# Kernel optimization log

Measured on AMD Instinct MI355X. Metric: run time of the kernel, lower is better.

The kernel has to match this reference:

```python
import jax, jax.numpy as jnp
import numpy as np

N = 62          # EEG channels (nodes per graph)
B = 512         # graphs in batch
K = 2           # SGConv propagation steps
F_IN = 128
H = 64
C = 3


def _complete_graph_edge_index():
    # edge e = g*N*N + i*N + j connects node g*N+i -> g*N+j,
    # matching edge_weight = Wsym.reshape(-1).repeat(B) ordering.
    base = np.arange(N)
    ii = np.tile(np.repeat(base, N), B)
    jj = np.tile(np.tile(base, N), B)
    off = np.repeat(np.arange(B) * N, N * N)
    return jnp.asarray(np.stack([off + ii, off + jj]).astype(np.int32))


def setup_inputs() -> dict:
    key = jax.random.key(0)
    ks = jax.random.split(key, 6)
    n_total = B * N
    x = jax.random.normal(ks[0], (n_total, F_IN), dtype=jnp.float32)
    edge_weight_tril = jax.random.normal(ks[1], (N * (N + 1) // 2,), dtype=jnp.float32)
    W1 = jax.random.normal(ks[2], (H, F_IN), dtype=jnp.float32) * (1.0 / np.sqrt(F_IN))
    b1 = jax.random.normal(ks[3], (H,), dtype=jnp.float32) * 0.01
    W2 = jax.random.normal(ks[4], (C, H), dtype=jnp.float32) * (1.0 / np.sqrt(H))
    b2 = jax.random.normal(ks[5], (C,), dtype=jnp.float32) * 0.01
    edge_index = _complete_graph_edge_index()
    batch = jnp.asarray(np.repeat(np.arange(B), N).astype(np.int32))
    return {"x": x, "edge_weight_tril": edge_weight_tril, "W1": W1, "b1": b1,
            "W2": W2, "b2": b2, "edge_index": edge_index, "batch": batch,
            "batch_size": B}


def reference(x, edge_weight_tril, W1, b1, W2, b2, edge_index, batch, batch_size):
    n_total = x.shape[0]
    # rebuild symmetric dense adjacency from lower-tri params
    xs, ys = np.tril_indices(N)
    Wm = jnp.zeros((N, N), dtype=x.dtype).at[xs, ys].set(edge_weight_tril)
    Wsym = Wm + Wm.T - jnp.diag(jnp.diag(Wm))
    ew = jnp.tile(Wsym.reshape(-1), batch_size)            # [B*N*N]

    row, col = edge_index[0], edge_index[1]
    # symmetric normalization (graph already contains self loops)
    deg = jax.ops.segment_sum(jnp.abs(ew), row, num_segments=n_total)
    dinv = jnp.where(deg > 0, deg ** -0.5, 0.0)
    norm = dinv[row] * ew * dinv[col]                      # [E]

    # K-step SGConv propagation: gather, scale, scatter-add
    h = x
    for _ in range(K):
        h = jax.ops.segment_sum(norm[:, None] * h[row], col, num_segments=n_total)

    h = jax.nn.relu(h @ W1.T + b1)                         # [n_total, H]
    pooled = jax.ops.segment_sum(h, batch, num_segments=batch_size)  # global_add_pool
    latent_v = pooled                                      # dropout in eval mode = identity
    logits = latent_v @ W2.T + b2
    logp = jax.nn.log_softmax(logits, axis=-1)
    return latent_v, logp
```

## Files before the change

kernel.cpp:

```cpp
#include <hip/hip_runtime.h>
#include <math.h>

#define NN  62
#define BGR 512
#define FIN 128
#define HD  64
#define NC  3

typedef __attribute__((ext_vector_type(8))) short          bf16x8;
typedef __attribute__((ext_vector_type(4))) float          f32x4;
typedef __attribute__((ext_vector_type(4))) unsigned short us4;

static __device__ __forceinline__ unsigned short f2bf(float f) {
    union { float f; unsigned u; } v; v.f = f;
    unsigned u = v.u;
    return (unsigned short)((u + 0x7fffu + ((u >> 16) & 1u)) >> 16);
}
static __device__ __forceinline__ float bf2f(unsigned short h) {
    union { unsigned u; float f; } v; v.u = ((unsigned)h) << 16;
    return v.f;
}

__global__ __launch_bounds__(512) void gcn_all(
    const float* __restrict__ x, const float* __restrict__ tril,
    const float* __restrict__ W1, const float* __restrict__ b1,
    const float* __restrict__ W2, const float* __restrict__ b2,
    float* __restrict__ out) {
    __shared__ unsigned short SH[45056];
    __shared__ float TAIL[2176 + 64 + 64];
    float* partial = TAIL;
    float* b1S     = TAIL + 2176;
    float* dinvS   = TAIL + 2240;

    const int t = threadIdx.x;
    const int gb = blockIdx.x;
    const int lane = t & 63, wv = t >> 6, quad = lane >> 4, l15 = lane & 15;
    const int w4 = wv & 3, gsel = wv >> 2;
    const int graph = 2 * gb + gsel;

    if (t < 16) *(float4*)&b1S[4 * t] = ((const float4*)b1)[t];

    bf16x8 xh[4], xl[4];
    {
        const int xr = 16 * w4 + l15;
        if (xr < NN) {
            const float* xrow = x + (size_t)graph * NN * FIN + (size_t)xr * FIN + quad * 8;
#pragma unroll
            for (int c = 0; c < 4; ++c) {
                float4 a = *(const float4*)(xrow + c * 32);
                float4 b = *(const float4*)(xrow + c * 32 + 4);
                float vv[8] = {a.x, a.y, a.z, a.w, b.x, b.y, b.z, b.w};
#pragma unroll
                for (int k = 0; k < 8; ++k) {
                    unsigned short h = f2bf(vv[k]);
                    xh[c][k] = (short)h;
                    xl[c][k] = (short)f2bf(vv[k] - bf2f(h));
                }
            }
        } else {
            bf16x8 zv = {0, 0, 0, 0, 0, 0, 0, 0};
#pragma unroll
            for (int c = 0; c < 4; ++c) { xh[c] = zv; xl[c] = zv; }
        }
    }

    const int arow_i = 16 * w4 + l15;
    const int jbase  = 16 * quad;
    float wreg[16];
    float dinv_r = 0.f;

    if (gsel == 1) {
        const float4* w14 = (const float4*)W1;
        for (int e = t - 256; e < 2048; e += 256) {
            int h = e >> 5, f4 = e & 31;
            float4 v = w14[e];
            us4 hh, ll;
            hh[0] = f2bf(v.x); ll[0] = f2bf(v.x - bf2f(hh[0]));
            hh[1] = f2bf(v.y); ll[1] = f2bf(v.y - bf2f(hh[1]));
            hh[2] = f2bf(v.z); ll[2] = f2bf(v.z - bf2f(hh[2]));
            hh[3] = f2bf(v.w); ll[3] = f2bf(v.w - bf2f(hh[3]));
            *(us4*)&SH[       h * 136 + f4 * 4] = hh;
            *(us4*)&SH[8704 + h * 136 + f4 * 4] = ll;
        }
    } else {
        float ps = 0.f;
#pragma unroll
        for (int jj = 0; jj < 16; ++jj) {
            int j = jbase + jj;
            float w = 0.f;
            if (arow_i < NN && j < NN) {
                int hi = arow_i > j ? arow_i : j;
                int lo = arow_i > j ? j : arow_i;
                w = tril[hi * (hi + 1) / 2 + lo];
            }
            wreg[jj] = w;
            ps += fabsf(w);
        }
        ps += __shfl_xor(ps, 16);
        ps += __shfl_xor(ps, 32);
        dinv_r = (ps > 0.f) ? (1.0f / sqrtf(ps)) : 0.f;
        if (lane < 16) dinvS[16 * w4 + lane] = dinv_r;
    }
    __syncthreads();

    if (gsel == 0) {
        const float di = dinv_r;
#pragma unroll
        for (int k = 0; k < 4; ++k) {
            float4 d4 = *(float4*)&dinvS[jbase + 4 * k];
            float dja[4] = {d4.x, d4.y, d4.z, d4.w};
            us4 hh, ll;
#pragma unroll
            for (int e = 0; e < 4; ++e) {
                float v = di * wreg[4 * k + e] * dja[e];
                hh[e] = f2bf(v);
                ll[e] = f2bf(v - bf2f(hh[e]));
            }
            *(us4*)&SH[17408 + arow_i * 72 + jbase + 4 * k] = hh;
            *(us4*)&SH[22016 + arow_i * 72 + jbase + 4 * k] = ll;
        }
    }
    __syncthreads();

    f32x4 za0 = {0,0,0,0}, za1 = {0,0,0,0};
    {
        const int arow = 17408 + arow_i * 72 + quad * 8;
        const int nt0 = 2 * gsel;
#pragma unroll
        for (int c = 0; c < 2; ++c) {
            bf16x8 ahi = *(bf16x8*)&SH[arow + c * 32];
            bf16x8 alo = *(bf16x8*)&SH[4608 + arow + c * 32];
#define ATILE(ACC, NT) { \
            int bo = 17408 + (16 * (NT) + l15) * 72 + quad * 8 + c * 32; \
            bf16x8 bhi = *(bf16x8*)&SH[bo]; \
            bf16x8 blo = *(bf16x8*)&SH[4608 + bo]; \
            ACC = __builtin_amdgcn_mfma_f32_16x16x32_bf16(ahi, bhi, ACC, 0, 0, 0); \
            ACC = __builtin_amdgcn_mfma_f32_16x16x32_bf16(ahi, blo, ACC, 0, 0, 0); \
            ACC = __builtin_amdgcn_mfma_f32_16x16x32_bf16(alo, bhi, ACC, 0, 0, 0); }
            ATILE(za0, nt0) ATILE(za1, nt0 + 1)
#undef ATILE
        }
    }

    f32x4 y0 = {0,0,0,0}, y1 = {0,0,0,0}, y2 = {0,0,0,0}, y3 = {0,0,0,0};
    {
#pragma unroll
        for (int c = 0; c < 4; ++c) {
            bf16x8 ahi = xh[c];
            bf16x8 alo = xl[c];
#define P1TILE(ACC, NT) { \
            int bo = (16 * (NT) + l15) * 136 + quad * 8 + c * 32; \
            bf16x8 bhi = *(bf16x8*)&SH[bo]; \
            bf16x8 blo = *(bf16x8*)&SH[8704 + bo]; \
            ACC = __builtin_amdgcn_mfma_f32_16x16x32_bf16(ahi, bhi, ACC, 0, 0, 0); \
            ACC = __builtin_amdgcn_mfma_f32_16x16x32_bf16(ahi, blo, ACC, 0, 0, 0); \
            ACC = __builtin_amdgcn_mfma_f32_16x16x32_bf16(alo, bhi, ACC, 0, 0, 0); }
            P1TILE(y0, 0) P1TILE(y1, 1) P1TILE(y2, 2) P1TILE(y3, 3)
#undef P1TILE
        }
    }
    __syncthreads();

    const int ytbase = 26624 + gsel * 9216;
    {
        const int mbase = 16 * w4 + quad * 4;
#define SPLITW(ACC, NT, HIOFF, LOOFF) { \
        int n = 16 * (NT) + l15; \
        us4 hh, ll; \
        hh[0] = f2bf(ACC[0]); ll[0] = f2bf(ACC[0] - bf2f(hh[0])); \
        hh[1] = f2bf(ACC[1]); ll[1] = f2bf(ACC[1] - bf2f(hh[1])); \
        hh[2] = f2bf(ACC[2]); ll[2] = f2bf(ACC[2] - bf2f(hh[2])); \
        hh[3] = f2bf(ACC[3]); ll[3] = f2bf(ACC[3] - bf2f(hh[3])); \
        *(us4*)&SH[(HIOFF) + n * 72 + mbase] = hh; \
        *(us4*)&SH[(LOOFF) + n * 72 + mbase] = ll; }
        SPLITW(y0, 0, ytbase, ytbase + 4608) SPLITW(y1, 1, ytbase, ytbase + 4608)
        SPLITW(y2, 2, ytbase, ytbase + 4608) SPLITW(y3, 3, ytbase, ytbase + 4608)
        SPLITW(za0, 2 * gsel,     17408, 22016)
        SPLITW(za1, 2 * gsel + 1, 17408, 22016)
#undef SPLITW
    }
    __syncthreads();

    f32x4 z0 = {0,0,0,0}, z1 = {0,0,0,0}, z2 = {0,0,0,0}, z3 = {0,0,0,0};
    {
        const int arow = 17408 + arow_i * 72 + quad * 8;
#pragma unroll
        for (int c = 0; c < 2; ++c) {
            bf16x8 ahi = *(bf16x8*)&SH[arow + c * 32];
            bf16x8 alo = *(bf16x8*)&SH[4608 + arow + c * 32];
#define P2TILE(ACC, NT) { \
            int bo = ytbase + (16 * (NT) + l15) * 72 + quad * 8 + c * 32; \
            bf16x8 bhi = *(bf16x8*)&SH[bo]; \
            bf16x8 blo = *(bf16x8*)&SH[4608 + bo]; \
            ACC = __builtin_amdgcn_mfma_f32_16x16x32_bf16(ahi, bhi, ACC, 0, 0, 0); \
            ACC = __builtin_amdgcn_mfma_f32_16x16x32_bf16(ahi, blo, ACC, 0, 0, 0); \
            ACC = __builtin_amdgcn_mfma_f32_16x16x32_bf16(alo, bhi, ACC, 0, 0, 0); }
            P2TILE(z0, 0) P2TILE(z1, 1) P2TILE(z2, 2) P2TILE(z3, 3)
#undef P2TILE
        }
    }

    {
        const int mbase = 16 * w4 + quad * 4;
        const int slot = 4 * w4 + quad;
        float* part = partial + gsel * 1088;
#define POOL(ACC, NT) { \
        int n = 16 * (NT) + l15; \
        float bn = b1S[n]; \
        float p = 0.f; \
        if (mbase + 0 < 62) p += fmaxf(ACC[0] + bn, 0.f); \
        if (mbase + 1 < 62) p += fmaxf(ACC[1] + bn, 0.f); \
        if (mbase + 2 < 62) p += fmaxf(ACC[2] + bn, 0.f); \
        if (mbase + 3 < 62) p += fmaxf(ACC[3] + bn, 0.f); \
        part[n * 17 + slot] = p; }
        POOL(z0, 0) POOL(z1, 1) POOL(z2, 2) POOL(z3, 3)
#undef POOL
    }
    __syncthreads();

    int tg = -1, tt = 0;
    if (t < 64)                    { tg = 0; tt = t; }
    else if (t >= 256 && t < 320)  { tg = 1; tt = t - 256; }
    if (tg >= 0) {
        const float* part = partial + tg * 1088;
        const int gr = 2 * gb + tg;
        float s = 0.f;
#pragma unroll
        for (int q = 0; q < 16; ++q) s += part[tt * 17 + q];
        out[(size_t)gr * HD + tt] = s;
        float l0 = s * W2[tt];
        float l1 = s * W2[64 + tt];
        float l2 = s * W2[128 + tt];
#pragma unroll
        for (int off = 32; off > 0; off >>= 1) {
            l0 += __shfl_down(l0, off);
            l1 += __shfl_down(l1, off);
            l2 += __shfl_down(l2, off);
        }
        if (tt == 0) {
            l0 += b2[0]; l1 += b2[1]; l2 += b2[2];
            float m = fmaxf(l0, fmaxf(l1, l2));
            float lse = m + logf(expf(l0 - m) + expf(l1 - m) + expf(l2 - m));
            float* lp = out + (size_t)BGR * HD + (size_t)gr * NC;
            lp[0] = l0 - lse; lp[1] = l1 - lse; lp[2] = l2 - lse;
        }
    }
}

extern "C" void kernel_launch(void* const* d_in, const int* in_sizes, int n_in,
                              void* d_out, int out_size, void* d_ws, size_t ws_size,
                              hipStream_t stream) {
    const float* x    = (const float*)d_in[0];
    const float* tril = (const float*)d_in[1];
    const float* W1   = (const float*)d_in[2];
    const float* b1   = (const float*)d_in[3];
    const float* W2   = (const float*)d_in[4];
    const float* b2   = (const float*)d_in[5];
    float* out = (float*)d_out;

    gcn_all<<<BGR / 2, 512, 0, stream>>>(x, tril, W1, b1, W2, b2, out);
}
```

Baseline: 92.88 us.

## Remove a barrier via separate normalized-adjacency buffer, defer x conversion, shuffle-reduce pool

The propagated adjacency now goes to a new LDS region instead of overwriting the normalized A tile. That removes the barrier between the second MFMA phase and the split-writes. The fp32-to-bf16 hi/lo split of x is deferred until after the adjacency/W1 staging, so the global loads can overlap with that work. Pooling partials are reduced across quads with wave shuffles, which replaces the 16-slot LDS reduction. LDS use grows by about 18 KB, which may lower occupancy.

```diff
diff --git a/kernel.cpp b/kernel.cpp
--- a/kernel.cpp
+++ b/kernel.cpp
@@ -26,11 +26,11 @@
     const float* __restrict__ W1, const float* __restrict__ b1,
     const float* __restrict__ W2, const float* __restrict__ b2,
     float* __restrict__ out) {
-    __shared__ unsigned short SH[45056];
-    __shared__ float TAIL[2176 + 64 + 64];
-    float* partial = TAIL;
-    float* b1S     = TAIL + 2176;
-    float* dinvS   = TAIL + 2240;
+    __shared__ unsigned short SH[54272];
+    __shared__ float TAIL[512 + 64 + 64];
+    float* partial2 = TAIL;
+    float* b1S      = TAIL + 512;
+    float* dinvS    = TAIL + 576;
 
     const int t = threadIdx.x;
     const int gb = blockIdx.x;
@@ -40,32 +40,35 @@
 
     if (t < 16) *(float4*)&b1S[4 * t] = ((const float4*)b1)[t];
 
+    const int arow_i = 16 * w4 + l15;
+    float4 xr4[8];
+    {
+        if (arow_i < NN) {
+            const float4* p4 = (const float4*)(x + (size_t)graph * NN * FIN
+                                               + (size_t)arow_i * FIN + quad * 8);
+#pragma unroll
+            for (int c = 0; c < 4; ++c) { xr4[2*c] = p4[8*c]; xr4[2*c+1] = p4[8*c+1]; }
+        } else {
+            float4 zz = {0.f, 0.f, 0.f, 0.f};
+#pragma unroll
+            for (int c = 0; c < 8; ++c) xr4[c] = zz;
+        }
+    }
     bf16x8 xh[4], xl[4];
-    {
-        const int xr = 16 * w4 + l15;
-        if (xr < NN) {
-            const float* xrow = x + (size_t)graph * NN * FIN + (size_t)xr * FIN + quad * 8;
-#pragma unroll
-            for (int c = 0; c < 4; ++c) {
-                float4 a = *(const float4*)(xrow + c * 32);
-                float4 b = *(const float4*)(xrow + c * 32 + 4);
-                float vv[8] = {a.x, a.y, a.z, a.w, b.x, b.y, b.z, b.w};
-#pragma unroll
-                for (int k = 0; k < 8; ++k) {
-                    unsigned short h = f2bf(vv[k]);
-                    xh[c][k] = (short)h;
-                    xl[c][k] = (short)f2bf(vv[k] - bf2f(h));
-                }
-            }
-        } else {
-            bf16x8 zv = {0, 0, 0, 0, 0, 0, 0, 0};
-#pragma unroll
-            for (int c = 0; c < 4; ++c) { xh[c] = zv; xl[c] = zv; }
-        }
-    }
-
-    const int arow_i = 16 * w4 + l15;
-    const int jbase  = 16 * quad;
+#define XCONV() { \
+    _Pragma("unroll") \
+    for (int c = 0; c < 4; ++c) { \
+        float vv[8] = {xr4[2*c].x, xr4[2*c].y, xr4[2*c].z, xr4[2*c].w, \
+                       xr4[2*c+1].x, xr4[2*c+1].y, xr4[2*c+1].z, xr4[2*c+1].w}; \
+        _Pragma("unroll") \
+        for (int k = 0; k < 8; ++k) { \
+            unsigned short h = f2bf(vv[k]); \
+            xh[c][k] = (short)h; \
+            xl[c][k] = (short)f2bf(vv[k] - bf2f(h)); \
+        } \
+    } }
+
+    const int jbase = 16 * quad;
     float wreg[16];
     float dinv_r = 0.f;
 
@@ -100,6 +103,7 @@
         ps += __shfl_xor(ps, 32);
         dinv_r = (ps > 0.f) ? (1.0f / sqrtf(ps)) : 0.f;
         if (lane < 16) dinvS[16 * w4 + lane] = dinv_r;
+        XCONV()
     }
     __syncthreads();
 
@@ -119,7 +123,10 @@
             *(us4*)&SH[17408 + arow_i * 72 + jbase + 4 * k] = hh;
             *(us4*)&SH[22016 + arow_i * 72 + jbase + 4 * k] = ll;
         }
-    }
+    } else {
+        XCONV()
+    }
+#undef XCONV
     __syncthreads();
 
     f32x4 za0 = {0,0,0,0}, za1 = {0,0,0,0};
@@ -159,9 +166,8 @@
 #undef P1TILE
         }
     }
-    __syncthreads();
-
-    const int ytbase = 26624 + gsel * 9216;
+
+    const int ytbase = 35840 + gsel * 9216;
     {
         const int mbase = 16 * w4 + quad * 4;
 #define SPLITW(ACC, NT, HIOFF, LOOFF) { \
@@ -175,15 +181,15 @@
         *(us4*)&SH[(LOOFF) + n * 72 + mbase] = ll; }
         SPLITW(y0, 0, ytbase, ytbase + 4608) SPLITW(y1, 1, ytbase, ytbase + 4608)
         SPLITW(y2, 2, ytbase, ytbase + 4608) SPLITW(y3, 3, ytbase, ytbase + 4608)
-        SPLITW(za0, 2 * gsel,     17408, 22016)
-        SPLITW(za1, 2 * gsel + 1, 17408, 22016)
+        SPLITW(za0, 2 * gsel,     26624, 31232)
+        SPLITW(za1, 2 * gsel + 1, 26624, 31232)
 #undef SPLITW
     }
     __syncthreads();
 
     f32x4 z0 = {0,0,0,0}, z1 = {0,0,0,0}, z2 = {0,0,0,0}, z3 = {0,0,0,0};
     {
-        const int arow = 17408 + arow_i * 72 + quad * 8;
+        const int arow = 26624 + arow_i * 72 + quad * 8;
 #pragma unroll
         for (int c = 0; c < 2; ++c) {
             bf16x8 ahi = *(bf16x8*)&SH[arow + c * 32];
@@ -202,8 +208,7 @@
 
     {
         const int mbase = 16 * w4 + quad * 4;
-        const int slot = 4 * w4 + quad;
-        float* part = partial + gsel * 1088;
+        float pv[4];
 #define POOL(ACC, NT) { \
         int n = 16 * (NT) + l15; \
         float bn = b1S[n]; \
@@ -212,9 +217,14 @@
         if (mbase + 1 < 62) p += fmaxf(ACC[1] + bn, 0.f); \
         if (mbase + 2 < 62) p += fmaxf(ACC[2] + bn, 0.f); \
         if (mbase + 3 < 62) p += fmaxf(ACC[3] + bn, 0.f); \
-        part[n * 17 + slot] = p; }
+        p += __shfl_xor(p, 16); \
+        p += __shfl_xor(p, 32); \
+        pv[NT] = p; }
         POOL(z0, 0) POOL(z1, 1) POOL(z2, 2) POOL(z3, 3)
 #undef POOL
+        float sel = (quad == 0) ? pv[0] : (quad == 1) ? pv[1]
+                  : (quad == 2) ? pv[2] : pv[3];
+        partial2[gsel * 256 + w4 * 64 + lane] = sel;
     }
     __syncthreads();
 
@@ -222,11 +232,9 @@
     if (t < 64)                    { tg = 0; tt = t; }
     else if (t >= 256 && t < 320)  { tg = 1; tt = t - 256; }
     if (tg >= 0) {
-        const float* part = partial + tg * 1088;
+        const float* part = partial2 + tg * 256;
         const int gr = 2 * gb + tg;
-        float s = 0.f;
-#pragma unroll
-        for (int q = 0; q < 16; ++q) s += part[tt * 17 + q];
+        float s = part[tt] + part[64 + tt] + part[128 + tt] + part[192 + tt];
         out[(size_t)gr * HD + tt] = s;
         float l0 = s * W2[tt];
         float l1 = s * W2[64 + tt];
```

Result: no change. 93.11 us (+0.2%).
